# Kernel tuning notes

Hardware: AMD Instinct MI355X
Metric: run time of the kernel (lower is better)

Reference implementation:

```python
import jax, jax.numpy as jnp
import numpy as np

P = 16
D = 768          # latent_dim
H = 3072         # hidden_dim
B = 256
OUT_DIMS = [100 + 10 * i for i in range(P)]   # sum = 2800
MAX_OUT = max(OUT_DIMS)
EPS = 1e-5


def setup_inputs() -> dict:
    key = jax.random.key(0)
    ks = jax.random.split(key, 6)
    x = jax.random.normal(ks[0], (B, P, D), dtype=jnp.float32)
    # LayerNorm params per part (torch default init: gamma=1, beta=0)
    gamma = jnp.ones((P, D), dtype=jnp.float32)
    beta = jnp.zeros((P, D), dtype=jnp.float32)
    # fc1: Linear(D, H, bias=False) per part -> stacked [P, H, D]
    w1 = jax.random.normal(ks[1], (P, H, D), dtype=jnp.float32) * 0.02
    # fc2: Linear(H, out_dims[i], bias=True) per part, padded to MAX_OUT.
    # Padded rows are never read (sliced away at concat).
    w2 = jax.random.normal(ks[2], (P, MAX_OUT, H), dtype=jnp.float32) * 0.02
    b2 = jnp.zeros((P, MAX_OUT), dtype=jnp.float32)
    return {"x": x, "gamma": gamma, "beta": beta, "w1": w1, "w2": w2, "b2": b2}


def reference(x, gamma, beta, w1, w2, b2):
    # Per-part LayerNorm over latent dim (torch uses biased variance)
    mu = jnp.mean(x, axis=-1, keepdims=True)
    var = jnp.mean(jnp.square(x - mu), axis=-1, keepdims=True)
    xn = (x - mu) * jax.lax.rsqrt(var + EPS) * gamma[None] + beta[None]  # [B,P,D]
    # fc1 (no bias) + exact GELU (torch.nn.GELU default)
    h = jnp.einsum('bpd,phd->bph', xn, w1)          # [B,P,H]
    h = jax.nn.gelu(h, approximate=False)
    # dropout p=0.0 -> identity
    # fc2 (with bias), padded grouped GEMM
    out_full = jnp.einsum('bph,poh->bpo', h, w2) + b2[None]  # [B,P,MAX_OUT]
    # concat variable-width slices along last dim
    out = jnp.concatenate([out_full[:, i, :OUT_DIMS[i]] for i in range(P)], axis=-1)
    return out  # [B, sum(OUT_DIMS)] = [256, 2800]
```

## Files before the change

kernel.cpp:

```cpp
#include <hip/hip_runtime.h>
#include <math.h>

typedef unsigned short u16;
typedef unsigned int u32;
typedef __attribute__((ext_vector_type(4))) float f32x4;
typedef __attribute__((ext_vector_type(8))) short bf16x8;

#define NP 16
#define DLAT 768
#define HDIM 3072
#define NB 256
#define MAXO 250
#define TOT 2800

__device__ __forceinline__ u16 f2b(float f) {
  union { float f; u32 u; } v; v.f = f;
  u32 u = v.u;
  u32 r = (u + 0x7fffu + ((u >> 16) & 1u)) >> 16;
  return (u16)r;
}

__device__ __forceinline__ u32 cvtpk(float lo, float hi) {
  u32 r;
  asm("v_cvt_pk_bf16_f32 %0, %1, %2" : "=v"(r) : "v"(lo), "v"(hi));
  return r;
}

__device__ __forceinline__ void gll16(const void* g, void* l) {
  __builtin_amdgcn_global_load_lds(
      (const __attribute__((address_space(1))) void*)g,
      (__attribute__((address_space(3))) void*)l, 16, 0, 0);
}

__global__ __launch_bounds__(256) void ln_kernel(
    const float* __restrict__ x, const float* __restrict__ gamma,
    const float* __restrict__ beta, u16* __restrict__ xn) {
  const int wave = threadIdx.x >> 6, lane = threadIdx.x & 63;
  const int row = blockIdx.x * 4 + wave;
  const int b = row >> 4, p = row & 15;
  const float4* xr = (const float4*)(x + (size_t)row * DLAT);
  const float4* g4 = (const float4*)(gamma + (size_t)p * DLAT);
  const float4* b4 = (const float4*)(beta + (size_t)p * DLAT);
  float4 v[3];
  float s = 0.f, ss = 0.f;
#pragma unroll
  for (int j = 0; j < 3; ++j) {
    v[j] = xr[lane + j * 64];
    s += v[j].x + v[j].y + v[j].z + v[j].w;
    ss += v[j].x * v[j].x + v[j].y * v[j].y + v[j].z * v[j].z + v[j].w * v[j].w;
  }
#pragma unroll
  for (int o = 32; o; o >>= 1) { s += __shfl_xor(s, o); ss += __shfl_xor(ss, o); }
  const float mu = s * (1.f / 768.f);
  const float var = ss * (1.f / 768.f) - mu * mu;
  const float rstd = rsqrtf(var + 1e-5f);
  u16* xo = xn + ((size_t)(p * NB + b)) * DLAT;
#pragma unroll
  for (int j = 0; j < 3; ++j) {
    const int f = lane + j * 64;
    float4 g = g4[f], be = b4[f];
    float o0 = (v[j].x - mu) * rstd * g.x + be.x;
    float o1 = (v[j].y - mu) * rstd * g.y + be.y;
    float o2 = (v[j].z - mu) * rstd * g.z + be.z;
    float o3 = (v[j].w - mu) * rstd * g.w + be.w;
    uint2 w;
    w.x = (u32)f2b(o0) | ((u32)f2b(o1) << 16);
    w.y = (u32)f2b(o2) | ((u32)f2b(o3) << 16);
    *(uint2*)&xo[f * 4] = w;
  }
}

__global__ __launch_bounds__(256, 5) void fc1_kernel(
    const u16* __restrict__ xn, const float* __restrict__ w1, u16* __restrict__ h) {
  const int bid = blockIdx.x;
  const int xcd = bid & 7;
  const int q = bid >> 3;
  const int g = xcd * 96 + (q >> 1);
  const int mb = q & 1;
  const int p = g / 48;
  const int n0 = (g % 48) * 64;
  const int m0 = mb * 128;

  const int tid = threadIdx.x;
  const int lane = tid & 63, wave = tid >> 6;
  const int lanelo = lane & 15, lanehi = lane >> 4;
  const int wr = wave >> 1, wc = wave & 1;

  const u16* Ap = xn + (size_t)p * NB * DLAT + (size_t)m0 * DLAT;
  const float* Bp = w1 + (size_t)p * HDIM * DLAT + (size_t)n0 * DLAT;

  __shared__ u16 AsU[2][128 * 32];
  __shared__ float BsF[2][64 * 32];

  int a_src[2], a_dst[2];
#pragma unroll
  for (int i = 0; i < 2; ++i) {
    const int s = wave * 128 + i * 64 + lane;
    const int r = s >> 2;
    const int gg = (s & 3) ^ ((r >> 1) & 3);
    a_src[i] = r * DLAT + gg * 8;
    a_dst[i] = (wave * 128 + i * 64) * 8;
  }
  int b_src[2], b_dst[2];
#pragma unroll
  for (int i = 0; i < 2; ++i) {
    const int s = wave * 128 + i * 64 + lane;
    const int r = s >> 3;
    const int gg = (s & 7) ^ (r & 7);
    b_src[i] = r * DLAT + gg * 4;
    b_dst[i] = (wave * 128 + i * 64) * 4;
  }
  int a_sl[4];
#pragma unroll
  for (int m = 0; m < 4; ++m) {
    const int ra = wr * 64 + m * 16 + lanelo;
    a_sl[m] = (ra * 4 + (lanehi ^ ((ra >> 1) & 3))) * 8;
  }
  int b_sl[2][2];
#pragma unroll
  for (int n = 0; n < 2; ++n) {
    const int rbl = wc * 32 + n * 16 + lanelo;
#pragma unroll
    for (int jj = 0; jj < 2; ++jj)
      b_sl[n][jj] = rbl * 32 + ((2 * lanehi + jj) ^ (rbl & 7)) * 4;
  }

  f32x4 acc[4][2] = {};
  const int NK = DLAT / 32;

  auto stage = [&](int kt) {
    const int k2 = kt * 32;
#pragma unroll
    for (int i = 0; i < 2; ++i)
      gll16(Ap + a_src[i] + k2, &AsU[kt & 1][a_dst[i]]);
#pragma unroll
    for (int i = 0; i < 2; ++i)
      gll16(Bp + b_src[i] + k2, &BsF[kt & 1][b_dst[i]]);
  };

  stage(0);
  __syncthreads();
#pragma unroll 2
  for (int kt = 0; kt < NK; ++kt) {
    const int cur = kt & 1;
    if (kt + 1 < NK) stage(kt + 1);
    const u16* a_ = &AsU[cur][0];
    const float* b_ = &BsF[cur][0];
    bf16x8 af[4], bf[2];
#pragma unroll
    for (int m = 0; m < 4; ++m) af[m] = *(const bf16x8*)&a_[a_sl[m]];
#pragma unroll
    for (int n = 0; n < 2; ++n) {
      const float4 f0 = *(const float4*)&b_[b_sl[n][0]];
      const float4 f1 = *(const float4*)&b_[b_sl[n][1]];
      union { u32 u[4]; bf16x8 v; } t;
      t.u[0] = cvtpk(f0.x, f0.y); t.u[1] = cvtpk(f0.z, f0.w);
      t.u[2] = cvtpk(f1.x, f1.y); t.u[3] = cvtpk(f1.z, f1.w);
      bf[n] = t.v;
    }
#pragma unroll
    for (int m = 0; m < 4; ++m)
#pragma unroll
      for (int n = 0; n < 2; ++n)
        acc[m][n] = __builtin_amdgcn_mfma_f32_16x16x32_bf16(af[m], bf[n], acc[m][n], 0, 0, 0);
    __syncthreads();
  }

  u16* hp = h + (size_t)p * NB * HDIM;
#pragma unroll
  for (int m = 0; m < 4; ++m) {
#pragma unroll
    for (int n = 0; n < 2; ++n) {
      const int col = n0 + wc * 32 + n * 16 + lanelo;
#pragma unroll
      for (int r = 0; r < 4; ++r) {
        const int row = m0 + wr * 64 + m * 16 + lanehi * 4 + r;
        const float vv = acc[m][n][r];
        const float gel = 0.5f * vv * (1.f + erff(vv * 0.70710678118654752f));
        hp[(size_t)row * HDIM + col] = f2b(gel);
      }
    }
  }
}

__global__ __launch_bounds__(256) void fc2_kernel(
    const u16* __restrict__ hbuf, const float* __restrict__ w2,
    const float* __restrict__ b2, float* __restrict__ out) {
  const int bid = blockIdx.x;
  const int bs = (bid & 7) * 32 + (bid >> 3);
  const int p = bs >> 4;
  const int mb = (bs >> 2) & 3;
  const int nb = bs & 3;
  const int odim = 100 + 10 * p;
  const int n0 = nb * 64;
  if (n0 >= odim) return;
  const int m0 = mb * 64;
  const int off = 100 * p + 5 * p * (p - 1);

  const int tid = threadIdx.x;
  const int lane = tid & 63, wave = tid >> 6;
  const int lanelo = lane & 15, lanehi = lane >> 4;
  const int wr = wave >> 1, wc = wave & 1;

  const u16* Ap = hbuf + (size_t)p * NB * HDIM + (size_t)m0 * HDIM;
  const float* Bp = w2 + (size_t)p * MAXO * HDIM;

  __shared__ u16 As[3][64 * 32];
  __shared__ u16 Bs[2][64 * 32];

  int ag_off;
  const int ag_base = (64 * wave) * 8;
  {
    int slot = 64 * wave + lane;
    int r = slot >> 2;
    int c = (slot & 3) ^ ((r >> 1) & 3);
    ag_off = r * HDIM + c * 8;
  }
  const int br0 = min(n0 + (tid >> 3), MAXO - 1);
  const int br1 = min(n0 + (tid >> 3) + 32, MAXO - 1);
  const float* bg0 = Bp + (size_t)br0 * HDIM + (tid & 7) * 4;
  const float* bg1 = Bp + (size_t)br1 * HDIM + (tid & 7) * 4;
  int bso[2];
#pragma unroll
  for (int i = 0; i < 2; ++i) {
    int r = (tid >> 3) + 32 * i;
    int c = ((tid & 7) >> 1) ^ ((r >> 1) & 3);
    bso[i] = (r * 4 + c) * 8 + (tid & 1) * 4;
  }
  int a_sl[2], b_sl[2];
#pragma unroll
  for (int m = 0; m < 2; ++m) {
    int r = wr * 32 + m * 16 + lanelo;
    a_sl[m] = (r * 4 + (lanehi ^ ((r >> 1) & 3))) * 8;
    int rb = wc * 32 + m * 16 + lanelo;
    b_sl[m] = (rb * 4 + (lanehi ^ ((rb >> 1) & 3))) * 8;
  }

  f32x4 acc[2][2] = {};
  float4 bA0, bA1, bB0, bB1;
  const int NK = HDIM / 32;

  auto issue = [&](int kt, float4& r0, float4& r1) {
    const int k2 = kt * 32;
    gll16(Ap + ag_off + k2, &As[kt % 3][ag_base]);
    asm volatile("" ::: "memory");
    r0 = *(const float4*)(bg0 + k2);
    r1 = *(const float4*)(bg1 + k2);
    asm volatile("" ::: "memory");
  };

  auto step = [&](int kt, float4& r0, float4& r1) {
    if (kt + 1 < NK) asm volatile("s_waitcnt vmcnt(3)" ::: "memory");
    else             asm volatile("s_waitcnt vmcnt(0)" ::: "memory");
    {
      u16* bb = &Bs[kt & 1][0];
      uint2 w0, w1v;
      w0.x = (u32)f2b(r0.x) | ((u32)f2b(r0.y) << 16);
      w0.y = (u32)f2b(r0.z) | ((u32)f2b(r0.w) << 16);
      w1v.x = (u32)f2b(r1.x) | ((u32)f2b(r1.y) << 16);
      w1v.y = (u32)f2b(r1.z) | ((u32)f2b(r1.w) << 16);
      *(uint2*)&bb[bso[0]] = w0;
      *(uint2*)&bb[bso[1]] = w1v;
    }
    asm volatile("s_waitcnt lgkmcnt(0)" ::: "memory");
    __builtin_amdgcn_s_barrier();
    asm volatile("" ::: "memory");
    if (kt + 2 < NK) issue(kt + 2, r0, r1);
    const u16* a_ = &As[kt % 3][0];
    const u16* b_ = &Bs[kt & 1][0];
    bf16x8 af[2], bf[2];
#pragma unroll
    for (int m = 0; m < 2; ++m) af[m] = *(const bf16x8*)&a_[a_sl[m]];
#pragma unroll
    for (int n = 0; n < 2; ++n) bf[n] = *(const bf16x8*)&b_[b_sl[n]];
#pragma unroll
    for (int m = 0; m < 2; ++m)
#pragma unroll
      for (int n = 0; n < 2; ++n)
        acc[m][n] = __builtin_amdgcn_mfma_f32_16x16x32_bf16(af[m], bf[n], acc[m][n], 0, 0, 0);
  };

  issue(0, bA0, bA1);
  issue(1, bB0, bB1);
  for (int kt = 0; kt < NK; kt += 2) {
    step(kt, bA0, bA1);
    step(kt + 1, bB0, bB1);
  }

#pragma unroll
  for (int m = 0; m < 2; ++m) {
#pragma unroll
    for (int n = 0; n < 2; ++n) {
      const int col = n0 + wc * 32 + n * 16 + lanelo;
      if (col < odim) {
        const float bias = b2[(size_t)p * MAXO + col];
#pragma unroll
        for (int r = 0; r < 4; ++r) {
          const int row = m0 + wr * 32 + m * 16 + lanehi * 4 + r;
          out[(size_t)row * TOT + off + col] = acc[m][n][r] + bias;
        }
      }
    }
  }
}

extern "C" void kernel_launch(void* const* d_in, const int* in_sizes, int n_in,
                              void* d_out, int out_size, void* d_ws, size_t ws_size,
                              hipStream_t stream) {
  const float* x = (const float*)d_in[0];
  const float* gamma = (const float*)d_in[1];
  const float* beta = (const float*)d_in[2];
  const float* w1 = (const float*)d_in[3];
  const float* w2 = (const float*)d_in[4];
  const float* b2 = (const float*)d_in[5];
  float* out = (float*)d_out;

  u16* xn = (u16*)d_ws;
  u16* h = (u16*)d_ws + (size_t)NP * NB * DLAT;

  ln_kernel<<<1024, 256, 0, stream>>>(x, gamma, beta, xn);
  fc1_kernel<<<1536, 256, 0, stream>>>(xn, w1, h);
  fc2_kernel<<<NP * 16, 256, 0, stream>>>(h, w2, b2, out);
}
```

Baseline: 106.5 us.

## Retile fc1 to 64x64 blocks with 128-wide K chunks and part-per-XCD mapping

Rewrites fc1 to use 64x64 output tiles (3072 blocks) instead of 128x64, and loads 128-wide K chunks per stage into single-buffered LDS in place of double-buffered 32-wide stages. Block-to-XCD mapping is changed so each XCD handles two whole parts, which should improve L2 reuse of the w1 and xn slices. The trade-off is that each fp32 w1 tile is now re-read by four M-blocks instead of two. Dropping the 5-waves occupancy hint and the double buffering gives up load/compute overlap in exchange for fewer barriers and larger transfers.

```diff
diff --git a/kernel.cpp b/kernel.cpp
--- a/kernel.cpp
+++ b/kernel.cpp
@@ -70,16 +70,16 @@
   }
 }
 
-__global__ __launch_bounds__(256, 5) void fc1_kernel(
+__global__ __launch_bounds__(256) void fc1_kernel(
     const u16* __restrict__ xn, const float* __restrict__ w1, u16* __restrict__ h) {
   const int bid = blockIdx.x;
   const int xcd = bid & 7;
-  const int q = bid >> 3;
-  const int g = xcd * 96 + (q >> 1);
-  const int mb = q & 1;
-  const int p = g / 48;
-  const int n0 = (g % 48) * 64;
-  const int m0 = mb * 128;
+  const int idx = bid >> 3;
+  const int p = xcd * 2 + (idx >= 192 ? 1 : 0);
+  const int r2 = idx % 192;
+  const int nb = r2 >> 2;
+  const int mb = r2 & 3;
+  const int m0 = mb * 64, n0 = nb * 64;
 
   const int tid = threadIdx.x;
   const int lane = tid & 63, wave = tid >> 6;
@@ -89,92 +89,75 @@
   const u16* Ap = xn + (size_t)p * NB * DLAT + (size_t)m0 * DLAT;
   const float* Bp = w1 + (size_t)p * HDIM * DLAT + (size_t)n0 * DLAT;
 
-  __shared__ u16 AsU[2][128 * 32];
-  __shared__ float BsF[2][64 * 32];
-
-  int a_src[2], a_dst[2];
-#pragma unroll
-  for (int i = 0; i < 2; ++i) {
-    const int s = wave * 128 + i * 64 + lane;
-    const int r = s >> 2;
-    const int gg = (s & 3) ^ ((r >> 1) & 3);
-    a_src[i] = r * DLAT + gg * 8;
-    a_dst[i] = (wave * 128 + i * 64) * 8;
-  }
-  int b_src[2], b_dst[2];
-#pragma unroll
-  for (int i = 0; i < 2; ++i) {
-    const int s = wave * 128 + i * 64 + lane;
-    const int r = s >> 3;
-    const int gg = (s & 7) ^ (r & 7);
-    b_src[i] = r * DLAT + gg * 4;
-    b_dst[i] = (wave * 128 + i * 64) * 4;
-  }
-  int a_sl[4];
-#pragma unroll
-  for (int m = 0; m < 4; ++m) {
-    const int ra = wr * 64 + m * 16 + lanelo;
-    a_sl[m] = (ra * 4 + (lanehi ^ ((ra >> 1) & 3))) * 8;
-  }
-  int b_sl[2][2];
-#pragma unroll
-  for (int n = 0; n < 2; ++n) {
-    const int rbl = wc * 32 + n * 16 + lanelo;
-#pragma unroll
-    for (int jj = 0; jj < 2; ++jj)
-      b_sl[n][jj] = rbl * 32 + ((2 * lanehi + jj) ^ (rbl & 7)) * 4;
-  }
-
-  f32x4 acc[4][2] = {};
-  const int NK = DLAT / 32;
-
-  auto stage = [&](int kt) {
-    const int k2 = kt * 32;
-#pragma unroll
-    for (int i = 0; i < 2; ++i)
-      gll16(Ap + a_src[i] + k2, &AsU[kt & 1][a_dst[i]]);
-#pragma unroll
-    for (int i = 0; i < 2; ++i)
-      gll16(Bp + b_src[i] + k2, &BsF[kt & 1][b_dst[i]]);
-  };
-
-  stage(0);
-  __syncthreads();
-#pragma unroll 2
-  for (int kt = 0; kt < NK; ++kt) {
-    const int cur = kt & 1;
-    if (kt + 1 < NK) stage(kt + 1);
-    const u16* a_ = &AsU[cur][0];
-    const float* b_ = &BsF[cur][0];
-    bf16x8 af[4], bf[2];
-#pragma unroll
-    for (int m = 0; m < 4; ++m) af[m] = *(const bf16x8*)&a_[a_sl[m]];
-#pragma unroll
-    for (int n = 0; n < 2; ++n) {
-      const float4 f0 = *(const float4*)&b_[b_sl[n][0]];
-      const float4 f1 = *(const float4*)&b_[b_sl[n][1]];
-      union { u32 u[4]; bf16x8 v; } t;
-      t.u[0] = cvtpk(f0.x, f0.y); t.u[1] = cvtpk(f0.z, f0.w);
-      t.u[2] = cvtpk(f1.x, f1.y); t.u[3] = cvtpk(f1.z, f1.w);
-      bf[n] = t.v;
+  __shared__ u16 As[64 * 128];
+  __shared__ float Bs[64 * 128];
+
+  int a_src[4], b_src[8];
+#pragma unroll
+  for (int j = 0; j < 4; ++j) {
+    const int s = tid + 256 * j;
+    const int r = s >> 4, c = s & 15;
+    a_src[j] = r * DLAT + ((c ^ (r & 7)) << 3);
+  }
+#pragma unroll
+  for (int j = 0; j < 8; ++j) {
+    const int s = tid + 256 * j;
+    const int r = s >> 5, c = s & 31;
+    b_src[j] = r * DLAT + ((c ^ (r & 7)) << 2);
+  }
+
+  const int ra0 = wr * 32 + lanelo;
+  const int rb0 = wc * 32 + lanelo;
+
+  f32x4 acc[2][2] = {};
+
+  for (int ch = 0; ch < 6; ++ch) {
+    const int k2 = ch * 128;
+#pragma unroll
+    for (int j = 0; j < 4; ++j)
+      gll16(Ap + a_src[j] + k2, &As[(tid + 256 * j) * 8]);
+#pragma unroll
+    for (int j = 0; j < 8; ++j)
+      gll16(Bp + b_src[j] + k2, &Bs[(tid + 256 * j) * 4]);
+    __syncthreads();
+#pragma unroll
+    for (int kt = 0; kt < 4; ++kt) {
+      bf16x8 af[2], bf[2];
+#pragma unroll
+      for (int m = 0; m < 2; ++m) {
+        const int ra = ra0 + m * 16;
+        af[m] = *(const bf16x8*)&As[ra * 128 + (((kt * 4 + lanehi) ^ (ra & 7)) << 3)];
+      }
+#pragma unroll
+      for (int n = 0; n < 2; ++n) {
+        const int rb = rb0 + n * 16;
+        const float4 f0 = *(const float4*)&Bs[rb * 128 + (((kt * 8 + lanehi * 2 + 0) ^ (rb & 7)) << 2)];
+        const float4 f1 = *(const float4*)&Bs[rb * 128 + (((kt * 8 + lanehi * 2 + 1) ^ (rb & 7)) << 2)];
+        union { u32 u[4]; bf16x8 v; } t;
+        t.u[0] = cvtpk(f0.x, f0.y);
+        t.u[1] = cvtpk(f0.z, f0.w);
+        t.u[2] = cvtpk(f1.x, f1.y);
+        t.u[3] = cvtpk(f1.z, f1.w);
+        bf[n] = t.v;
+      }
+#pragma unroll
+      for (int m = 0; m < 2; ++m)
+#pragma unroll
+        for (int n = 0; n < 2; ++n)
+          acc[m][n] = __builtin_amdgcn_mfma_f32_16x16x32_bf16(af[m], bf[n], acc[m][n], 0, 0, 0);
     }
-#pragma unroll
-    for (int m = 0; m < 4; ++m)
-#pragma unroll
-      for (int n = 0; n < 2; ++n)
-        acc[m][n] = __builtin_amdgcn_mfma_f32_16x16x32_bf16(af[m], bf[n], acc[m][n], 0, 0, 0);
     __syncthreads();
   }
 
   u16* hp = h + (size_t)p * NB * HDIM;
 #pragma unroll
-  for (int m = 0; m < 4; ++m) {
+  for (int m = 0; m < 2; ++m) {
 #pragma unroll
     for (int n = 0; n < 2; ++n) {
       const int col = n0 + wc * 32 + n * 16 + lanelo;
 #pragma unroll
       for (int r = 0; r < 4; ++r) {
-        const int row = m0 + wr * 64 + m * 16 + lanehi * 4 + r;
+        const int row = m0 + wr * 32 + m * 16 + lanehi * 4 + r;
         const float vv = acc[m][n][r];
         const float gel = 0.5f * vv * (1.f + erff(vv * 0.70710678118654752f));
         hp[(size_t)row * HDIM + col] = f2b(gel);
@@ -319,6 +302,6 @@
   u16* h = (u16*)d_ws + (size_t)NP * NB * DLAT;
 
   ln_kernel<<<1024, 256, 0, stream>>>(x, gamma, beta, xn);
-  fc1_kernel<<<1536, 256, 0, stream>>>(xn, w1, h);
+  fc1_kernel<<<3072, 256, 0, stream>>>(xn, w1, h);
   fc2_kernel<<<NP * 16, 256, 0, stream>>>(h, w2, b2, out);
 }
```

New measurement: 103.6 us. 1.03x faster.
